# Performance work log

Hardware: AMD Instinct MI355X
Metric: run time of the kernel (lower is better)

Reference implementation:

```python
import jax, jax.numpy as jnp
import numpy as np

B, N, R = 4, 64, 8          # batch, num nodes, num resources
D, H, E = 32, 96, 2         # node_dim_in, hidden_dim (=3*D), edge_dim_out
PSTEP = 2


def setup_inputs() -> dict:
    key = jax.random.key(0)
    ks = jax.random.split(key, 24)
    g = lambda k, shape: (jax.random.normal(k, shape, dtype=jnp.float32) * 0.05)
    z = lambda n: jnp.zeros((n,), dtype=jnp.float32)
    return {
        "node_rep": jax.random.normal(ks[0], (B, N, R, D), dtype=jnp.float32),
        # node_encoder: Linear(D->H), ReLU
        "ne_W": g(ks[1], (D, H)), "ne_b": z(H),
        # edge_encoder: Linear(2D->H), ReLU  (edge_dim_in == 0)
        "ee_W": g(ks[2], (2 * D, H)), "ee_b": z(H),
        # node_propagator: Linear(3H->H), ReLU, Linear(H->H), ReLU
        "np_W1": g(ks[3], (3 * H, H)), "np_b1": z(H),
        "np_W2": g(ks[4], (H, H)), "np_b2": z(H),
        # edge_propagators (pstep=2), each Linear(3H->H),ReLU,Linear(H->H),ReLU
        "ep0_W1": g(ks[5], (3 * H, H)), "ep0_b1": z(H),
        "ep0_W2": g(ks[6], (H, H)), "ep0_b2": z(H),
        "ep1_W1": g(ks[7], (3 * H, H)), "ep1_b1": z(H),
        "ep1_W2": g(ks[8], (H, H)), "ep1_b2": z(H),
        # edge_predictor: Linear(2H->H), ReLU, Linear(H->E)
        "pred_W1": g(ks[9], (2 * H, H)), "pred_b1": z(H),
        "pred_W2": g(ks[10], (H, E)), "pred_b2": z(E),
    }


def _propnet_edge_fwd(node_rep, ne_W, ne_b, ee_W, ee_b,
                      np_W1, np_b1, np_W2, np_b2,
                      ep_params, pred_W1, pred_b1, pred_W2, pred_b2):
    relu = jax.nn.relu
    d = node_rep.shape[-1]
    h = ne_W.shape[-1]

    # node encoder: [B,N,R,H]
    node_enc = relu(node_rep @ ne_W + ne_b)

    # edge encoder on cat([receiver, sender]); split the weight so we never
    # materialize the [B,N,N,R,2D] concat (Linear(cat) == r@Wr + s@Ws + b).
    Wr, Ws = ee_W[:d], ee_W[d:]
    # receiver varies along axis 1, sender along axis 2 -> [B,N,N,R,H]
    edge_enc = relu((node_rep @ Wr)[:, :, None] + (node_rep @ Ws)[:, None, :] + ee_b)

    node_effect, edge_effect = node_enc, edge_enc
    Wn1, Wn2, Wn3 = np_W1[:h], np_W1[h:2 * h], np_W1[2 * h:]
    for (W1, b1, W2, b2) in ep_params:
        Er, Es, Ee = W1[:h], W1[h:2 * h], W1[2 * h:]
        t = relu((node_effect @ Er)[:, :, None]
                 + (node_effect @ Es)[:, None, :]
                 + edge_effect @ Ee + b1)
        edge_effect = relu(t @ W2 + b2)                      # [B,N,N,R,H]
        edge_effect_agg = edge_effect.sum(axis=2)             # sum over senders -> [B,N,R,H]
        t = relu(node_enc @ Wn1 + node_effect @ Wn2 + edge_effect_agg @ Wn3 + np_b1)
        node_effect = relu(t @ np_W2 + np_b2)                 # [B,N,R,H]

    # edge predictor on cat([edge_effect, edge_enc]) with split weights
    Pe, Pc = pred_W1[:h], pred_W1[h:]
    t = relu(edge_effect @ Pe + edge_enc @ Pc + pred_b1)
    edge_pred = t @ pred_W2 + pred_b2                         # [B,N,N,R,E]
    return edge_pred


def reference(node_rep, ne_W, ne_b, ee_W, ee_b,
              np_W1, np_b1, np_W2, np_b2,
              ep0_W1, ep0_b1, ep0_W2, ep0_b2,
              ep1_W1, ep1_b1, ep1_W2, ep1_b2,
              pred_W1, pred_b1, pred_W2, pred_b2):
    ep_params = [(ep0_W1, ep0_b1, ep0_W2, ep0_b2),
                 (ep1_W1, ep1_b1, ep1_W2, ep1_b2)]
    return _propnet_edge_fwd(node_rep, ne_W, ne_b, ee_W, ee_b,
                             np_W1, np_b1, np_W2, np_b2,
                             ep_params, pred_W1, pred_b1, pred_W2, pred_b2)
```

## Files before the change

### kernel.cpp

```cpp
#include <hip/hip_runtime.h>
#include <hip/hip_bf16.h>

#define BB 4
#define NN 64
#define RR 8
#define DD 32
#define HH 96
#define NGROUP (BB*NN*RR)
#define LSTR 17

#define OFF_WR_T  0
#define OFF_WS_T  196608
#define OFF_NER0  393216
#define OFF_NES0  589824
#define OFF_NER1  786432
#define OFF_NES1  983040
#define OFF_ENCT  1179648
#define OFF_AGGT  1376256
#define OFF_PKE   1572864
#define OFF_PKN   1601280
#define OFF_EE0F  1675008

#define PE_EE0  0
#define PE_W20  4608
#define PE_EE1  9216
#define PE_W21  13824
#define PE_PE   18432
#define PE_PC   23040
#define PE_P2   27648
#define PN_NEW  0
#define PN_WR   3072
#define PN_WS   6144
#define PN_ER0  9216
#define PN_ES0  18432
#define PN_WN12 27648
#define PN_WN3  36864
#define PN_NPW2 46080
#define PN_ER1  55296
#define PN_ES1  64512

typedef __attribute__((ext_vector_type(4))) float f32x4;
typedef __attribute__((ext_vector_type(8))) short bf16x8;
typedef __attribute__((ext_vector_type(4))) unsigned int u32x4;

__device__ __forceinline__ unsigned int pk2(float lo, float hi){
    unsigned short a = __builtin_bit_cast(unsigned short, __float2bfloat16(lo));
    unsigned short b = __builtin_bit_cast(unsigned short, __float2bfloat16(hi));
    return (unsigned)a | ((unsigned)b << 16);
}
__device__ __forceinline__ void split2(float v0, float v1, unsigned &h, unsigned &lo){
    float h0 = __bfloat162float(__float2bfloat16(v0));
    float h1 = __bfloat162float(__float2bfloat16(v1));
    h  = pk2(v0, v1);
    lo = pk2(v0 - h0, v1 - h1);
}

#define MFMA16(A,B,C) __builtin_amdgcn_mfma_f32_16x16x32_bf16((A),(B),(C),0,0,0)

__device__ __forceinline__ void gemm_1m(f32x4 &acc,
    const unsigned* __restrict__ ph, const unsigned* __restrict__ pl,
    int idx, int l, const u32x4 &Bh, const u32x4 &Bl)
{
    bf16x8 bh = __builtin_bit_cast(bf16x8, Bh);
    bf16x8 bl = __builtin_bit_cast(bf16x8, Bl);
    bf16x8 ah = __builtin_bit_cast(bf16x8, *(const u32x4*)&ph[idx*256 + l*4]);
    bf16x8 al = __builtin_bit_cast(bf16x8, *(const u32x4*)&pl[idx*256 + l*4]);
    acc = MFMA16(ah, bh, acc);
    acc = MFMA16(ah, bl, acc);
    acc = MFMA16(al, bh, acc);
}
__device__ __forceinline__ void buildB_lds(const float* sF, int kb, int gq, int cL,
                                           u32x4 &Bh, u32x4 &Bl){
    #pragma unroll
    for (int p=0;p<4;p++){
        int f = 32*kb + 8*gq + 2*p;
        unsigned h, lo;
        split2(sF[f*LSTR + cL], sF[(f+1)*LSTR + cL], h, lo);
        Bh[p] = h; Bl[p] = lo;
    }
}
__device__ __forceinline__ void gemm96_1m(f32x4 &acc,
    const unsigned* __restrict__ ph, const unsigned* __restrict__ pl,
    int w, int l, int gq, int cL, const float* sF)
{
    #pragma unroll
    for (int kb=0;kb<3;kb++){
        u32x4 Bh, Bl;
        buildB_lds(sF, kb, gq, cL, Bh, Bl);
        gemm_1m(acc, ph, pl, w*3+kb, l, Bh, Bl);
    }
}
__device__ __forceinline__ void relu1(f32x4 &acc){
    #pragma unroll
    for (int q=0;q<4;q++) acc[q] = fmaxf(acc[q], 0.f);
}
__device__ __forceinline__ void cinit1(f32x4 &acc, const float* __restrict__ bv, int w, int gq){
    #pragma unroll
    for (int q=0;q<4;q++) acc[q] = bv[16*w+4*gq+q];
}
__device__ __forceinline__ void storeT1(const f32x4 &acc, float* __restrict__ dst,
                                        int w, int gq, int col){
    #pragma unroll
    for (int q=0;q<4;q++) dst[(16*w+4*gq+q)*NN + col] = acc[q];
}
__device__ __forceinline__ void toLds1(const f32x4 &acc, float* sF, int w, int gq, int cL){
    #pragma unroll
    for (int q=0;q<4;q++) sF[(16*w+4*gq+q)*LSTR + cL] = acc[q];
}

__device__ __forceinline__ void einit_b(f32x4 (&acc)[3][4], const float* __restrict__ bv,
                                        int mBase, int gq){
    #pragma unroll
    for (int mi=0;mi<3;mi++)
      #pragma unroll
      for (int q=0;q<4;q++){
        float x = bv[16*(mBase+mi)+4*gq+q];
        #pragma unroll
        for (int n=0;n<4;n++) acc[mi][n][q] = x;
      }
}
__device__ __forceinline__ void egemm_kb(f32x4 (&acc)[3][4],
    const unsigned* __restrict__ Apk, int mBase, int kb, int l, const u32x4 (&Bk)[4])
{
    #pragma unroll
    for (int mi=0;mi<3;mi++){
        bf16x8 a = __builtin_bit_cast(bf16x8, *(const u32x4*)&Apk[(((mBase+mi)*3+kb)*64 + l)*4]);
        #pragma unroll
        for (int n=0;n<4;n++){
            bf16x8 bf = __builtin_bit_cast(bf16x8, Bk[n]);
            acc[mi][n] = MFMA16(a, bf, acc[mi][n]);
        }
    }
}
__device__ __forceinline__ void build_ee_kb(u32x4 (&Bk)[4],
    const float* __restrict__ wrt, const float* __restrict__ wst,
    int i, int kb, int gq, int cL)
{
    #pragma unroll
    for (int n=0;n<4;n++)
      #pragma unroll
      for (int p=0;p<4;p++){
        int h = 32*kb + 8*gq + 2*p;
        int j = 16*n + cL;
        float a0 = fmaxf(wrt[h*NN + i]     + wst[h*NN + j],     0.f);
        float a1 = fmaxf(wrt[(h+1)*NN + i] + wst[(h+1)*NN + j], 0.f);
        Bk[n][p] = pk2(a0, a1);
      }
}
__device__ __forceinline__ void load_sB_kb(u32x4 (&Bk)[4], const unsigned* sB, int kb, int l){
    #pragma unroll
    for (int n=0;n<4;n++) Bk[n] = *(const u32x4*)&sB[((kb*4+n)*64 + l)*4];
}
__device__ __forceinline__ void repack_half(const f32x4 (&acc)[3][4], unsigned* sB,
                                            int mBase, int gq, int cL)
{
    #pragma unroll
    for (int mi=0;mi<3;mi++){
      int m = mBase+mi;
      #pragma unroll
      for (int n=0;n<4;n++){
        float v0 = fmaxf(acc[mi][n][0],0.f), v1 = fmaxf(acc[mi][n][1],0.f);
        float v2 = fmaxf(acc[mi][n][2],0.f), v3 = fmaxf(acc[mi][n][3],0.f);
        int gd = 2*(m&1) + (gq>>1);
        int dw = (((m>>1)*4 + n)*64 + 16*gd + cL)*4 + 2*(gq&1);
        sB[dw]   = pk2(v0,v1);
        sB[dw+1] = pk2(v2,v3);
      }
    }
}

__global__ __launch_bounds__(64)
void k0_pack(const float* __restrict__ ne_W, const float* __restrict__ ee_W,
             const float* __restrict__ ep0_W1, const float* __restrict__ ep0_W2,
             const float* __restrict__ ep1_W1, const float* __restrict__ ep1_W2,
             const float* __restrict__ np_W1, const float* __restrict__ np_W2,
             const float* __restrict__ pred_W1, const float* __restrict__ pred_W2,
             unsigned* __restrict__ pk_e, unsigned* __restrict__ pk_n)
{
    int t = blockIdx.x, l = threadIdx.x;
    int cL = l & 15, gq = l >> 4;
    if (t < 108) {
        int mat = t/18, tt = t%18, mt = tt/3, kb = tt%3;
        const float* mats[6] = { ep0_W1 + 2*HH*HH, ep0_W2, ep1_W1 + 2*HH*HH,
                                 ep1_W2, pred_W1, pred_W1 + HH*HH };
        const float* src = mats[mat];
        u32x4 d;
        #pragma unroll
        for (int p=0;p<4;p++){
            int k = 32*kb + 8*gq + 2*p;
            d[p] = pk2(src[k*HH + 16*mt + cL], src[(k+1)*HH + 16*mt + cL]);
        }
        *(u32x4*)&pk_e[mat*4608 + (mt*3+kb)*256 + l*4] = d;
    } else if (t < 111) {
        int kb = t - 108;
        u32x4 d;
        #pragma unroll
        for (int p=0;p<4;p++){
            int k = 32*kb + 8*gq + 2*p;
            float lo = (cL < 2) ? pred_W2[k*2 + cL]     : 0.f;
            float hi = (cL < 2) ? pred_W2[(k+1)*2 + cL] : 0.f;
            d[p] = pk2(lo, hi);
        }
        *(u32x4*)&pk_e[PE_P2 + kb*256 + l*4] = d;
    } else {
        int u = t - 111;
        if (u < 18) {
            int mat = u/6, mt = u%6;
            const float* srcs[3] = { ne_W, ee_W, ee_W + DD*HH };
            const float* src = srcs[mat];
            u32x4 dh, dl;
            #pragma unroll
            for (int p=0;p<4;p++){
                int k = 8*gq + 2*p;
                unsigned th, tl;
                split2(src[k*HH + 16*mt + cL], src[(k+1)*HH + 16*mt + cL], th, tl);
                dh[p] = th; dl[p] = tl;
            }
            int base = mat*3072 + mt*256 + l*4;
            *(u32x4*)&pk_n[base]        = dh;
            *(u32x4*)&pk_n[base + 1536] = dl;
        } else {
            int u2 = u-18, mat = u2/18, tt = u2%18, mt = tt/3, kb = tt%3;
            u32x4 dh, dl;
            #pragma unroll
            for (int p=0;p<4;p++){
                int k = 32*kb + 8*gq + 2*p, col = 16*mt + cL;
                float v0, v1;
                if (mat == 2) {
                    v0 = np_W1[k*HH+col]     + np_W1[(HH+k)*HH+col];
                    v1 = np_W1[(k+1)*HH+col] + np_W1[(HH+k+1)*HH+col];
                } else {
                    const float* src = (mat==0) ? ep0_W1
                                     : (mat==1) ? ep0_W1 + HH*HH
                                     : (mat==3) ? np_W1 + 2*HH*HH
                                     : (mat==4) ? np_W2
                                     : (mat==5) ? ep1_W1
                                     :            ep1_W1 + HH*HH;
                    v0 = src[k*HH+col]; v1 = src[(k+1)*HH+col];
                }
                unsigned th, tl;
                split2(v0, v1, th, tl);
                dh[p] = th; dl[p] = tl;
            }
            int base = PN_ER0 + mat*9216 + (mt*3+kb)*256 + l*4;
            *(u32x4*)&pk_n[base]        = dh;
            *(u32x4*)&pk_n[base + 4608] = dl;
        }
    }
}

__global__ __launch_bounds__(384)
void k1_node(const float* __restrict__ node_rep,
             const float* __restrict__ ne_b, const float* __restrict__ ee_b,
             const float* __restrict__ ep0_b1,
             const unsigned* __restrict__ pk_n,
             float* __restrict__ wr_t, float* __restrict__ ws_t,
             float* __restrict__ ner0_t, float* __restrict__ nes0_t,
             float* __restrict__ enc_t)
{
    int blk = blockIdx.x, tid = threadIdx.x;
    int br = blk >> 2, chunk = blk & 3;
    int b = br >> 3, r = br & 7;
    int w = tid >> 6, l = tid & 63;
    int cL = l & 15, gq = l >> 4;
    int col = 16*chunk + cL;
    __shared__ float sN[DD*16];
    __shared__ __align__(16) float sF[HH*LSTR];
    size_t brb = (size_t)br * HH * NN;

    for (int idx = tid; idx < 512; idx += 384){
        int row = idx >> 5, k = idx & 31;
        sN[k*16 + row] = node_rep[((size_t)((b*NN + 16*chunk + row)*RR + r))*DD + k];
    }
    __syncthreads();

    u32x4 nBh, nBl;
    #pragma unroll
    for (int p=0;p<4;p++){
        int k = 8*gq + 2*p;
        unsigned h, lo;
        split2(sN[k*16 + cL], sN[(k+1)*16 + cL], h, lo);
        nBh[p] = h; nBl[p] = lo;
    }

    f32x4 acc;

    cinit1(acc, ne_b, w, gq);
    gemm_1m(acc, pk_n+PN_NEW, pk_n+PN_NEW+1536, w, l, nBh, nBl);
    relu1(acc);
    storeT1(acc, enc_t + brb, w, gq, col);
    toLds1(acc, sF, w, gq, cL);
    __syncthreads();

    cinit1(acc, ep0_b1, w, gq);
    gemm96_1m(acc, pk_n+PN_ER0, pk_n+PN_ER0+4608, w, l, gq, cL, sF);
    storeT1(acc, ner0_t + brb, w, gq, col);

    #pragma unroll
    for (int q=0;q<4;q++) acc[q] = 0.f;
    gemm96_1m(acc, pk_n+PN_ES0, pk_n+PN_ES0+4608, w, l, gq, cL, sF);
    storeT1(acc, nes0_t + brb, w, gq, col);

    cinit1(acc, ee_b, w, gq);
    gemm_1m(acc, pk_n+PN_WR, pk_n+PN_WR+1536, w, l, nBh, nBl);
    storeT1(acc, wr_t + brb, w, gq, col);

    #pragma unroll
    for (int q=0;q<4;q++) acc[q] = 0.f;
    gemm_1m(acc, pk_n+PN_WS, pk_n+PN_WS+1536, w, l, nBh, nBl);
    storeT1(acc, ws_t + brb, w, gq, col);
}

__global__ __launch_bounds__(128)
void k2_edge0(const float* __restrict__ wr_t, const float* __restrict__ ws_t,
              const float* __restrict__ ner0_t, const float* __restrict__ nes0_t,
              const unsigned* __restrict__ pk_e,
              const float* __restrict__ ep0_b2,
              unsigned* __restrict__ ee0f, float* __restrict__ agg_t)
{
    int g = blockIdx.x, tid = threadIdx.x;
    int w = tid >> 6, l = tid & 63;
    int b = g >> 9, r = g & 7, i = (g >> 3) & 63;
    int cL = l & 15, gq = l >> 4;
    int mBase = 3*w;
    size_t brb = (size_t)(b*RR + r)*HH*NN;
    const float* wrt = wr_t   + brb;
    const float* nrt = ner0_t + brb;
    const float* wst = ws_t   + brb;
    const float* nst = nes0_t + brb;
    __shared__ __align__(16) unsigned sB[3072];

    f32x4 acc[3][4];
    #pragma unroll
    for (int mi=0;mi<3;mi++)
      #pragma unroll
      for (int q=0;q<4;q++){
        int c = 16*(mBase+mi) + 4*gq + q;
        float nr = nrt[c*NN + i];
        #pragma unroll
        for (int n=0;n<4;n++) acc[mi][n][q] = nr + nst[c*NN + 16*n + cL];
      }

    #pragma unroll
    for (int kb=0;kb<3;kb++){
        u32x4 Bk[4];
        build_ee_kb(Bk, wrt, wst, i, kb, gq, cL);
        egemm_kb(acc, pk_e + PE_EE0, mBase, kb, l, Bk);
    }
    repack_half(acc, sB, mBase, gq, cL);
    __syncthreads();

    einit_b(acc, ep0_b2, mBase, gq);
    #pragma unroll
    for (int kb=0;kb<3;kb++){
        u32x4 Bk[4];
        load_sB_kb(Bk, sB, kb, l);
        egemm_kb(acc, pk_e + PE_W20, mBase, kb, l, Bk);
    }
    #pragma unroll
    for (int mi=0;mi<3;mi++)
      #pragma unroll
      for (int n=0;n<4;n++)
        #pragma unroll
        for (int q=0;q<4;q++) acc[mi][n][q] = fmaxf(acc[mi][n][q], 0.f);

    unsigned* eo = ee0f + (size_t)g*3072;
    #pragma unroll
    for (int mi=0;mi<3;mi++){
      int m = mBase+mi;
      #pragma unroll
      for (int n=0;n<4;n++){
        int gd = 2*(m&1) + (gq>>1);
        int dw = (((m>>1)*4 + n)*64 + 16*gd + cL)*4 + 2*(gq&1);
        eo[dw]   = pk2(acc[mi][n][0], acc[mi][n][1]);
        eo[dw+1] = pk2(acc[mi][n][2], acc[mi][n][3]);
      }
    }
    #pragma unroll
    for (int mi=0;mi<3;mi++)
      #pragma unroll
      for (int q=0;q<4;q++){
        float s = acc[mi][0][q] + acc[mi][1][q] + acc[mi][2][q] + acc[mi][3][q];
        s += __shfl_xor(s, 1);
        s += __shfl_xor(s, 2);
        s += __shfl_xor(s, 4);
        s += __shfl_xor(s, 8);
        if (cL == 0) agg_t[brb + (16*(mBase+mi) + 4*gq + q)*NN + i] = s;
      }
}

__global__ __launch_bounds__(384)
void k3_node(const float* __restrict__ enc_t_g, const float* __restrict__ agg_t_g,
             const float* __restrict__ np_b1, const float* __restrict__ np_b2,
             const float* __restrict__ ep1_b1,
             const unsigned* __restrict__ pk_n,
             float* __restrict__ ner1_t, float* __restrict__ nes1_t)
{
    int blk = blockIdx.x, tid = threadIdx.x;
    int br = blk >> 2, chunk = blk & 3;
    int w = tid >> 6, l = tid & 63;
    int cL = l & 15, gq = l >> 4;
    int col = 16*chunk + cL;
    __shared__ __align__(16) float sE[HH*LSTR], sA[HH*LSTR], sF[HH*LSTR];
    size_t brb = (size_t)br * HH * NN;
    const float* enc_t = enc_t_g + brb;
    const float* agg_t = agg_t_g + brb;

    for (int idx = tid; idx < HH*16; idx += 384){
        int f = idx >> 4, c = idx & 15;
        sE[f*LSTR + c] = enc_t[f*NN + 16*chunk + c];
        sA[f*LSTR + c] = agg_t[f*NN + 16*chunk + c];
    }
    __syncthreads();

    f32x4 acc;

    cinit1(acc, np_b1, w, gq);
    gemm96_1m(acc, pk_n+PN_WN12, pk_n+PN_WN12+4608, w, l, gq, cL, sE);
    gemm96_1m(acc, pk_n+PN_WN3,  pk_n+PN_WN3+4608,  w, l, gq, cL, sA);
    relu1(acc);
    toLds1(acc, sF, w, gq, cL);
    __syncthreads();

    cinit1(acc, np_b2, w, gq);
    gemm96_1m(acc, pk_n+PN_NPW2, pk_n+PN_NPW2+4608, w, l, gq, cL, sF);
    relu1(acc);
    __syncthreads();
    toLds1(acc, sF, w, gq, cL);
    __syncthreads();

    cinit1(acc, ep1_b1, w, gq);
    gemm96_1m(acc, pk_n+PN_ER1, pk_n+PN_ER1+4608, w, l, gq, cL, sF);
    storeT1(acc, ner1_t + brb, w, gq, col);

    #pragma unroll
    for (int q=0;q<4;q++) acc[q] = 0.f;
    gemm96_1m(acc, pk_n+PN_ES1, pk_n+PN_ES1+4608, w, l, gq, cL, sF);
    storeT1(acc, nes1_t + brb, w, gq, col);
}

__global__ __launch_bounds__(128)
void k4_edge1(const float* __restrict__ wr_t, const float* __restrict__ ws_t,
              const float* __restrict__ ner1_t, const float* __restrict__ nes1_t,
              const unsigned* __restrict__ pk_e,
              const unsigned* __restrict__ ee0f,
              const float* __restrict__ ep1_b2,
              const float* __restrict__ pred_b1, const float* __restrict__ pred_b2,
              float* __restrict__ out)
{
    int g = blockIdx.x, tid = threadIdx.x;
    int w = tid >> 6, l = tid & 63;
    int b = g >> 9, i = (g >> 3) & 63, r = g & 7;
    int cL = l & 15, gq = l >> 4;
    int mBase = 3*w;
    size_t brb = (size_t)(b*RR + r)*HH*NN;
    const float* wrt = wr_t   + brb;
    const float* wst = ws_t   + brb;
    const float* nrt = ner1_t + brb;
    const float* nst = nes1_t + brb;
    __shared__ __align__(16) unsigned sB[3072];

    const u32x4* e0p = (const u32x4*)ee0f + (size_t)g*768;

    f32x4 acc[3][4];
    #pragma unroll
    for (int mi=0;mi<3;mi++)
      #pragma unroll
      for (int q=0;q<4;q++){
        int c = 16*(mBase+mi) + 4*gq + q;
        float nr = nrt[c*NN + i];
        #pragma unroll
        for (int n=0;n<4;n++) acc[mi][n][q] = nr + nst[c*NN + 16*n + cL];
      }

    #pragma unroll
    for (int kb=0;kb<3;kb++){
        u32x4 Bk[4];
        #pragma unroll
        for (int n=0;n<4;n++) Bk[n] = e0p[(kb*4+n)*64 + l];
        egemm_kb(acc, pk_e + PE_EE1, mBase, kb, l, Bk);
    }
    repack_half(acc, sB, mBase, gq, cL);
    __syncthreads();

    einit_b(acc, ep1_b2, mBase, gq);
    #pragma unroll
    for (int kb=0;kb<3;kb++){
        u32x4 Bk[4];
        load_sB_kb(Bk, sB, kb, l);
        egemm_kb(acc, pk_e + PE_W21, mBase, kb, l, Bk);
    }
    __syncthreads();
    repack_half(acc, sB, mBase, gq, cL);
    __syncthreads();

    einit_b(acc, pred_b1, mBase, gq);
    #pragma unroll
    for (int kb=0;kb<3;kb++){
        u32x4 Bk[4];
        load_sB_kb(Bk, sB, kb, l);
        egemm_kb(acc, pk_e + PE_PE, mBase, kb, l, Bk);
    }
    __syncthreads();

    #pragma unroll
    for (int kb=0;kb<3;kb++){
        u32x4 Bk[4];
        build_ee_kb(Bk, wrt, wst, i, kb, gq, cL);
        egemm_kb(acc, pk_e + PE_PC, mBase, kb, l, Bk);
    }
    repack_half(acc, sB, mBase, gq, cL);
    __syncthreads();

    f32x4 c5[2];
    #pragma unroll
    for (int nn=0;nn<2;nn++){
        c5[nn][0] = (gq == 0) ? pred_b2[0] : 0.f;
        c5[nn][1] = (gq == 0) ? pred_b2[1] : 0.f;
        c5[nn][2] = 0.f; c5[nn][3] = 0.f;
    }
    #pragma unroll
    for (int kb=0;kb<3;kb++){
        bf16x8 A2 = __builtin_bit_cast(bf16x8, *(const u32x4*)&pk_e[PE_P2 + (kb*64 + l)*4]);
        #pragma unroll
        for (int nn=0;nn<2;nn++){
            int n = 2*w + nn;
            bf16x8 Bf = __builtin_bit_cast(bf16x8, *(const u32x4*)&sB[((kb*4+n)*64 + l)*4]);
            c5[nn] = MFMA16(A2, Bf, c5[nn]);
        }
    }
    if (gq == 0) {
        float2* o2 = (float2*)out;
        #pragma unroll
        for (int nn=0;nn<2;nn++){
            size_t j = 16*(2*w+nn) + cL;
            o2[(((size_t)(b*NN + i))*NN + j)*RR + r] = make_float2(c5[nn][0], c5[nn][1]);
        }
    }
}

extern "C" void kernel_launch(void* const* d_in, const int* in_sizes, int n_in,
                              void* d_out, int out_size, void* d_ws, size_t ws_size,
                              hipStream_t stream)
{
    const float* node_rep = (const float*)d_in[0];
    const float* ne_W    = (const float*)d_in[1];
    const float* ne_b    = (const float*)d_in[2];
    const float* ee_W    = (const float*)d_in[3];
    const float* ee_b    = (const float*)d_in[4];
    const float* np_W1   = (const float*)d_in[5];
    const float* np_b1   = (const float*)d_in[6];
    const float* np_W2   = (const float*)d_in[7];
    const float* np_b2   = (const float*)d_in[8];
    const float* ep0_W1  = (const float*)d_in[9];
    const float* ep0_b1  = (const float*)d_in[10];
    const float* ep0_W2  = (const float*)d_in[11];
    const float* ep0_b2  = (const float*)d_in[12];
    const float* ep1_W1  = (const float*)d_in[13];
    const float* ep1_b1  = (const float*)d_in[14];
    const float* ep1_W2  = (const float*)d_in[15];
    const float* ep1_b2  = (const float*)d_in[16];
    const float* pred_W1 = (const float*)d_in[17];
    const float* pred_b1 = (const float*)d_in[18];
    const float* pred_W2 = (const float*)d_in[19];
    const float* pred_b2 = (const float*)d_in[20];
    float* wsf = (float*)d_ws;
    float* out = (float*)d_out;

    float* wr_t   = wsf + OFF_WR_T;
    float* ws_t   = wsf + OFF_WS_T;
    float* ner0_t = wsf + OFF_NER0;
    float* nes0_t = wsf + OFF_NES0;
    float* ner1_t = wsf + OFF_NER1;
    float* nes1_t = wsf + OFF_NES1;
    float* enc_t  = wsf + OFF_ENCT;
    float* agg_t  = wsf + OFF_AGGT;
    unsigned* pk_e = (unsigned*)(wsf + OFF_PKE);
    unsigned* pk_n = (unsigned*)(wsf + OFF_PKN);
    unsigned* ee0f = (unsigned*)(wsf + OFF_EE0F);

    k0_pack<<<255, 64, 0, stream>>>(ne_W, ee_W, ep0_W1, ep0_W2, ep1_W1, ep1_W2,
                                    np_W1, np_W2, pred_W1, pred_W2, pk_e, pk_n);

    k1_node<<<128, 384, 0, stream>>>(node_rep, ne_b, ee_b, ep0_b1, pk_n,
                                     wr_t, ws_t, ner0_t, nes0_t, enc_t);

    k2_edge0<<<NGROUP, 128, 0, stream>>>(wr_t, ws_t, ner0_t, nes0_t, pk_e, ep0_b2,
                                         ee0f, agg_t);

    k3_node<<<128, 384, 0, stream>>>(enc_t, agg_t, np_b1, np_b2, ep1_b1, pk_n,
                                     ner1_t, nes1_t);

    k4_edge1<<<NGROUP, 128, 0, stream>>>(wr_t, ws_t, ner1_t, nes1_t, pk_e, ee0f,
                                         ep1_b2, pred_b1, pred_b2, out);
}
```

Baseline: 68.73 us.

## Split edge kernels across six waves with one M-tile per wave

The edge kernels k2 and k4 now launch 384 threads per block (six wavefronts) instead of 128. Each wave owns a single 16-row M-tile instead of three, which shrinks accumulator register pressure and raises the number of waves available to hide latency. In exchange, each wave redundantly rebuilds the edge-encoding B operand and reloads B fragments from LDS, and block-wide barriers now synchronise six waves. The final predictor step uses only four of the six waves.

```diff
diff --git a/kernel.cpp b/kernel.cpp
--- a/kernel.cpp
+++ b/kernel.cpp
@@ -108,28 +108,23 @@
     for (int q=0;q<4;q++) sF[(16*w+4*gq+q)*LSTR + cL] = acc[q];
 }
 
-__device__ __forceinline__ void einit_b(f32x4 (&acc)[3][4], const float* __restrict__ bv,
-                                        int mBase, int gq){
-    #pragma unroll
-    for (int mi=0;mi<3;mi++)
-      #pragma unroll
-      for (int q=0;q<4;q++){
-        float x = bv[16*(mBase+mi)+4*gq+q];
-        #pragma unroll
-        for (int n=0;n<4;n++) acc[mi][n][q] = x;
-      }
-}
-__device__ __forceinline__ void egemm_kb(f32x4 (&acc)[3][4],
-    const unsigned* __restrict__ Apk, int mBase, int kb, int l, const u32x4 (&Bk)[4])
-{
-    #pragma unroll
-    for (int mi=0;mi<3;mi++){
-        bf16x8 a = __builtin_bit_cast(bf16x8, *(const u32x4*)&Apk[(((mBase+mi)*3+kb)*64 + l)*4]);
-        #pragma unroll
-        for (int n=0;n<4;n++){
-            bf16x8 bf = __builtin_bit_cast(bf16x8, Bk[n]);
-            acc[mi][n] = MFMA16(a, bf, acc[mi][n]);
-        }
+__device__ __forceinline__ void einit1(f32x4 (&acc)[4], const float* __restrict__ bv,
+                                       int m, int gq){
+    #pragma unroll
+    for (int q=0;q<4;q++){
+        float x = bv[16*m+4*gq+q];
+        #pragma unroll
+        for (int n=0;n<4;n++) acc[n][q] = x;
+    }
+}
+__device__ __forceinline__ void egemm1_kb(f32x4 (&acc)[4],
+    const unsigned* __restrict__ Apk, int m, int kb, int l, const u32x4 (&Bk)[4])
+{
+    bf16x8 a = __builtin_bit_cast(bf16x8, *(const u32x4*)&Apk[((m*3+kb)*64 + l)*4]);
+    #pragma unroll
+    for (int n=0;n<4;n++){
+        bf16x8 bf = __builtin_bit_cast(bf16x8, Bk[n]);
+        acc[n] = MFMA16(a, bf, acc[n]);
     }
 }
 __device__ __forceinline__ void build_ee_kb(u32x4 (&Bk)[4],
@@ -151,21 +146,17 @@
     #pragma unroll
     for (int n=0;n<4;n++) Bk[n] = *(const u32x4*)&sB[((kb*4+n)*64 + l)*4];
 }
-__device__ __forceinline__ void repack_half(const f32x4 (&acc)[3][4], unsigned* sB,
-                                            int mBase, int gq, int cL)
-{
-    #pragma unroll
-    for (int mi=0;mi<3;mi++){
-      int m = mBase+mi;
-      #pragma unroll
-      for (int n=0;n<4;n++){
-        float v0 = fmaxf(acc[mi][n][0],0.f), v1 = fmaxf(acc[mi][n][1],0.f);
-        float v2 = fmaxf(acc[mi][n][2],0.f), v3 = fmaxf(acc[mi][n][3],0.f);
+__device__ __forceinline__ void repack_one(const f32x4 (&acc)[4], unsigned* sB,
+                                           int m, int gq, int cL)
+{
+    #pragma unroll
+    for (int n=0;n<4;n++){
+        float v0 = fmaxf(acc[n][0],0.f), v1 = fmaxf(acc[n][1],0.f);
+        float v2 = fmaxf(acc[n][2],0.f), v3 = fmaxf(acc[n][3],0.f);
         int gd = 2*(m&1) + (gq>>1);
         int dw = (((m>>1)*4 + n)*64 + 16*gd + cL)*4 + 2*(gq&1);
         sB[dw]   = pk2(v0,v1);
         sB[dw+1] = pk2(v2,v3);
-      }
     }
 }
 
@@ -311,7 +302,7 @@
     storeT1(acc, ws_t + brb, w, gq, col);
 }
 
-__global__ __launch_bounds__(128)
+__global__ __launch_bounds__(384)
 void k2_edge0(const float* __restrict__ wr_t, const float* __restrict__ ws_t,
               const float* __restrict__ ner0_t, const float* __restrict__ nes0_t,
               const unsigned* __restrict__ pk_e,
@@ -322,7 +313,6 @@
     int w = tid >> 6, l = tid & 63;
     int b = g >> 9, r = g & 7, i = (g >> 3) & 63;
     int cL = l & 15, gq = l >> 4;
-    int mBase = 3*w;
     size_t brb = (size_t)(b*RR + r)*HH*NN;
     const float* wrt = wr_t   + brb;
     const float* nrt = ner0_t + brb;
@@ -330,63 +320,53 @@
     const float* nst = nes0_t + brb;
     __shared__ __align__(16) unsigned sB[3072];
 
-    f32x4 acc[3][4];
-    #pragma unroll
-    for (int mi=0;mi<3;mi++)
-      #pragma unroll
-      for (int q=0;q<4;q++){
-        int c = 16*(mBase+mi) + 4*gq + q;
+    f32x4 acc[4];
+    #pragma unroll
+    for (int q=0;q<4;q++){
+        int c = 16*w + 4*gq + q;
         float nr = nrt[c*NN + i];
         #pragma unroll
-        for (int n=0;n<4;n++) acc[mi][n][q] = nr + nst[c*NN + 16*n + cL];
-      }
+        for (int n=0;n<4;n++) acc[n][q] = nr + nst[c*NN + 16*n + cL];
+    }
 
     #pragma unroll
     for (int kb=0;kb<3;kb++){
         u32x4 Bk[4];
         build_ee_kb(Bk, wrt, wst, i, kb, gq, cL);
-        egemm_kb(acc, pk_e + PE_EE0, mBase, kb, l, Bk);
-    }
-    repack_half(acc, sB, mBase, gq, cL);
-    __syncthreads();
-
-    einit_b(acc, ep0_b2, mBase, gq);
+        egemm1_kb(acc, pk_e + PE_EE0, w, kb, l, Bk);
+    }
+    repack_one(acc, sB, w, gq, cL);
+    __syncthreads();
+
+    einit1(acc, ep0_b2, w, gq);
     #pragma unroll
     for (int kb=0;kb<3;kb++){
         u32x4 Bk[4];
         load_sB_kb(Bk, sB, kb, l);
-        egemm_kb(acc, pk_e + PE_W20, mBase, kb, l, Bk);
-    }
-    #pragma unroll
-    for (int mi=0;mi<3;mi++)
+        egemm1_kb(acc, pk_e + PE_W20, w, kb, l, Bk);
+    }
+    #pragma unroll
+    for (int n=0;n<4;n++)
       #pragma unroll
-      for (int n=0;n<4;n++)
-        #pragma unroll
-        for (int q=0;q<4;q++) acc[mi][n][q] = fmaxf(acc[mi][n][q], 0.f);
+      for (int q=0;q<4;q++) acc[n][q] = fmaxf(acc[n][q], 0.f);
 
     unsigned* eo = ee0f + (size_t)g*3072;
     #pragma unroll
-    for (int mi=0;mi<3;mi++){
-      int m = mBase+mi;
-      #pragma unroll
-      for (int n=0;n<4;n++){
-        int gd = 2*(m&1) + (gq>>1);
-        int dw = (((m>>1)*4 + n)*64 + 16*gd + cL)*4 + 2*(gq&1);
-        eo[dw]   = pk2(acc[mi][n][0], acc[mi][n][1]);
-        eo[dw+1] = pk2(acc[mi][n][2], acc[mi][n][3]);
-      }
-    }
-    #pragma unroll
-    for (int mi=0;mi<3;mi++)
-      #pragma unroll
-      for (int q=0;q<4;q++){
-        float s = acc[mi][0][q] + acc[mi][1][q] + acc[mi][2][q] + acc[mi][3][q];
+    for (int n=0;n<4;n++){
+        int gd = 2*(w&1) + (gq>>1);
+        int dw = (((w>>1)*4 + n)*64 + 16*gd + cL)*4 + 2*(gq&1);
+        eo[dw]   = pk2(acc[n][0], acc[n][1]);
+        eo[dw+1] = pk2(acc[n][2], acc[n][3]);
+    }
+    #pragma unroll
+    for (int q=0;q<4;q++){
+        float s = acc[0][q] + acc[1][q] + acc[2][q] + acc[3][q];
         s += __shfl_xor(s, 1);
         s += __shfl_xor(s, 2);
         s += __shfl_xor(s, 4);
         s += __shfl_xor(s, 8);
-        if (cL == 0) agg_t[brb + (16*(mBase+mi) + 4*gq + q)*NN + i] = s;
-      }
+        if (cL == 0) agg_t[brb + (16*w + 4*gq + q)*NN + i] = s;
+    }
 }
 
 __global__ __launch_bounds__(384)
@@ -439,7 +419,7 @@
     storeT1(acc, nes1_t + brb, w, gq, col);
 }
 
-__global__ __launch_bounds__(128)
+__global__ __launch_bounds__(384)
 void k4_edge1(const float* __restrict__ wr_t, const float* __restrict__ ws_t,
               const float* __restrict__ ner1_t, const float* __restrict__ nes1_t,
               const unsigned* __restrict__ pk_e,
@@ -452,7 +432,6 @@
     int w = tid >> 6, l = tid & 63;
     int b = g >> 9, i = (g >> 3) & 63, r = g & 7;
     int cL = l & 15, gq = l >> 4;
-    int mBase = 3*w;
     size_t brb = (size_t)(b*RR + r)*HH*NN;
     const float* wrt = wr_t   + brb;
     const float* wst = ws_t   + brb;
@@ -462,44 +441,42 @@
 
     const u32x4* e0p = (const u32x4*)ee0f + (size_t)g*768;
 
-    f32x4 acc[3][4];
-    #pragma unroll
-    for (int mi=0;mi<3;mi++)
-      #pragma unroll
-      for (int q=0;q<4;q++){
-        int c = 16*(mBase+mi) + 4*gq + q;
+    f32x4 acc[4];
+    #pragma unroll
+    for (int q=0;q<4;q++){
+        int c = 16*w + 4*gq + q;
         float nr = nrt[c*NN + i];
         #pragma unroll
-        for (int n=0;n<4;n++) acc[mi][n][q] = nr + nst[c*NN + 16*n + cL];
-      }
+        for (int n=0;n<4;n++) acc[n][q] = nr + nst[c*NN + 16*n + cL];
+    }
 
     #pragma unroll
     for (int kb=0;kb<3;kb++){
         u32x4 Bk[4];
         #pragma unroll
         for (int n=0;n<4;n++) Bk[n] = e0p[(kb*4+n)*64 + l];
-        egemm_kb(acc, pk_e + PE_EE1, mBase, kb, l, Bk);
-    }
-    repack_half(acc, sB, mBase, gq, cL);
-    __syncthreads();
-
-    einit_b(acc, ep1_b2, mBase, gq);
+        egemm1_kb(acc, pk_e + PE_EE1, w, kb, l, Bk);
+    }
+    repack_one(acc, sB, w, gq, cL);
+    __syncthreads();
+
+    einit1(acc, ep1_b2, w, gq);
     #pragma unroll
     for (int kb=0;kb<3;kb++){
         u32x4 Bk[4];
         load_sB_kb(Bk, sB, kb, l);
-        egemm_kb(acc, pk_e + PE_W21, mBase, kb, l, Bk);
-    }
-    __syncthreads();
-    repack_half(acc, sB, mBase, gq, cL);
-    __syncthreads();
-
-    einit_b(acc, pred_b1, mBase, gq);
+        egemm1_kb(acc, pk_e + PE_W21, w, kb, l, Bk);
+    }
+    __syncthreads();
+    repack_one(acc, sB, w, gq, cL);
+    __syncthreads();
+
+    einit1(acc, pred_b1, w, gq);
     #pragma unroll
     for (int kb=0;kb<3;kb++){
         u32x4 Bk[4];
         load_sB_kb(Bk, sB, kb, l);
-        egemm_kb(acc, pk_e + PE_PE, mBase, kb, l, Bk);
+        egemm1_kb(acc, pk_e + PE_PE, w, kb, l, Bk);
     }
     __syncthreads();
 
@@ -507,34 +484,26 @@
     for (int kb=0;kb<3;kb++){
         u32x4 Bk[4];
         build_ee_kb(Bk, wrt, wst, i, kb, gq, cL);
-        egemm_kb(acc, pk_e + PE_PC, mBase, kb, l, Bk);
-    }
-    repack_half(acc, sB, mBase, gq, cL);
-    __syncthreads();
-
-    f32x4 c5[2];
-    #pragma unroll
-    for (int nn=0;nn<2;nn++){
-        c5[nn][0] = (gq == 0) ? pred_b2[0] : 0.f;
-        c5[nn][1] = (gq == 0) ? pred_b2[1] : 0.f;
-        c5[nn][2] = 0.f; c5[nn][3] = 0.f;
-    }
-    #pragma unroll
-    for (int kb=0;kb<3;kb++){
-        bf16x8 A2 = __builtin_bit_cast(bf16x8, *(const u32x4*)&pk_e[PE_P2 + (kb*64 + l)*4]);
-        #pragma unroll
-        for (int nn=0;nn<2;nn++){
-            int n = 2*w + nn;
-            bf16x8 Bf = __builtin_bit_cast(bf16x8, *(const u32x4*)&sB[((kb*4+n)*64 + l)*4]);
-            c5[nn] = MFMA16(A2, Bf, c5[nn]);
+        egemm1_kb(acc, pk_e + PE_PC, w, kb, l, Bk);
+    }
+    repack_one(acc, sB, w, gq, cL);
+    __syncthreads();
+
+    if (w < 4) {
+        f32x4 c5;
+        c5[0] = (gq == 0) ? pred_b2[0] : 0.f;
+        c5[1] = (gq == 0) ? pred_b2[1] : 0.f;
+        c5[2] = 0.f; c5[3] = 0.f;
+        #pragma unroll
+        for (int kb=0;kb<3;kb++){
+            bf16x8 A2 = __builtin_bit_cast(bf16x8, *(const u32x4*)&pk_e[PE_P2 + (kb*64 + l)*4]);
+            bf16x8 Bf = __builtin_bit_cast(bf16x8, *(const u32x4*)&sB[((kb*4+w)*64 + l)*4]);
+            c5 = MFMA16(A2, Bf, c5);
         }
-    }
-    if (gq == 0) {
-        float2* o2 = (float2*)out;
-        #pragma unroll
-        for (int nn=0;nn<2;nn++){
-            size_t j = 16*(2*w+nn) + cL;
-            o2[(((size_t)(b*NN + i))*NN + j)*RR + r] = make_float2(c5[nn][0], c5[nn][1]);
+        if (gq == 0) {
+            float2* o2 = (float2*)out;
+            size_t j = 16*w + cL;
+            o2[(((size_t)(b*NN + i))*NN + j)*RR + r] = make_float2(c5[0], c5[1]);
         }
     }
 }
@@ -585,12 +554,12 @@
     k1_node<<<128, 384, 0, stream>>>(node_rep, ne_b, ee_b, ep0_b1, pk_n,
                                      wr_t, ws_t, ner0_t, nes0_t, enc_t);
 
-    k2_edge0<<<NGROUP, 128, 0, stream>>>(wr_t, ws_t, ner0_t, nes0_t, pk_e, ep0_b2,
+    k2_edge0<<<NGROUP, 384, 0, stream>>>(wr_t, ws_t, ner0_t, nes0_t, pk_e, ep0_b2,
                                          ee0f, agg_t);
 
     k3_node<<<128, 384, 0, stream>>>(enc_t, agg_t, np_b1, np_b2, ep1_b1, pk_n,
                                      ner1_t, nes1_t);
 
-    k4_edge1<<<NGROUP, 128, 0, stream>>>(wr_t, ws_t, ner1_t, nes1_t, pk_e, ee0f,
+    k4_edge1<<<NGROUP, 384, 0, stream>>>(wr_t, ws_t, ner1_t, nes1_t, pk_e, ee0f,
                                          ep1_b2, pred_b1, pred_b2, out);
 }
```

Result: slower. 87.00 us (+26.6%).
